# Kernel tuning notes

Hardware: AMD Instinct MI355X
Metric: run time of the kernel (lower is better)

## Reference

```python
import math
import jax, jax.numpy as jnp
import numpy as np

PRED_LEN = 96
K = 32
LOW_FREQ = 1


def setup_inputs() -> dict:
    key = jax.random.key(0)
    x = jax.random.normal(key, (8, 512, 512), dtype=jnp.float32)
    return {"x": x}


def _fourier_forward(x):
    b, t, d = x.shape
    # rFFT over time axis (always fp32, matching torch autocast-disabled block)
    x_freq = jnp.fft.rfft(x.astype(jnp.float32), axis=1)  # (b, t//2+1, d) complex64
    freqs = jnp.fft.rfftfreq(t).astype(jnp.float32)
    if t % 2 == 0:
        x_freq = x_freq[:, LOW_FREQ:-1]
        f = freqs[LOW_FREQ:-1]
    else:
        x_freq = x_freq[:, LOW_FREQ:]
        f = freqs[LOW_FREQ:]
    n_freq = x_freq.shape[1]
    k = min(K, n_freq)

    # top-k |X(f)| independently per (batch, channel): move freq to last axis
    mag = jnp.transpose(jnp.abs(x_freq), (0, 2, 1))          # (b, d, f)
    _, idx = jax.lax.top_k(mag, k)                            # (b, d, k)
    x_freq_t = jnp.transpose(x_freq, (0, 2, 1))               # (b, d, f)
    x_sel = jnp.transpose(jnp.take_along_axis(x_freq_t, idx, axis=2), (0, 2, 1))  # (b, k, d)
    f_sel = jnp.transpose(f[idx], (0, 2, 1))[:, :, None, :]   # (b, k, 1, d)

    # extrapolate: add conjugate (negative) frequencies
    x_full = jnp.concatenate([x_sel, jnp.conj(x_sel)], axis=1)  # (b, 2k, d)
    f_full = jnp.concatenate([f_sel, -f_sel], axis=1)           # (b, 2k, 1, d)
    t_val = jnp.arange(t + PRED_LEN, dtype=jnp.float32)[None, None, :, None]  # (1,1,T,1)
    amp = (jnp.abs(x_full) / t)[:, :, None, :]                  # (b, 2k, 1, d)
    phase = jnp.angle(x_full)[:, :, None, :]                    # (b, 2k, 1, d)
    x_time = amp * jnp.cos(2.0 * math.pi * f_full * t_val + phase)  # (b, 2k, T, d)
    return jnp.sum(x_time, axis=1)                              # (b, t+pred_len, d)


def reference(x):
    return _fourier_forward(x)
```

## Files before the change

### kernel.cpp

```cpp
#include <hip/hip_runtime.h>
#include <math.h>

#define BATCH 8
#define TLEN  512
#define DDIM  512
#define TOUT  608
#define KSEL  32
#define DT    8

#define TWO_PI_OVER_512 0.0122718463030851562f
#define SC (2.0f / 512.0f)

typedef __attribute__((ext_vector_type(8))) short short8;
typedef __attribute__((ext_vector_type(4))) float f32x4;

#define BMT_OFF 0
#define WK_OFF  4194304

__device__ __forceinline__ unsigned short f2bf(float f) {
    unsigned u = __float_as_uint(f);
    return (unsigned short)((u + 0x7FFF + ((u >> 16) & 1)) >> 16);
}

__device__ __constant__ const float CC16[16] = {
     1.f,  0.92387953251128674f,  0.70710678118654752f,  0.38268343236508977f,
     0.f, -0.38268343236508977f, -0.70710678118654752f, -0.92387953251128674f,
    -1.f, -0.92387953251128674f, -0.70710678118654752f, -0.38268343236508977f,
     0.f,  0.38268343236508977f,  0.70710678118654752f,  0.92387953251128674f };
__device__ __constant__ const float SS16[16] = {
     0.f,  0.38268343236508977f,  0.70710678118654752f,  0.92387953251128674f,
     1.f,  0.92387953251128674f,  0.70710678118654752f,  0.38268343236508977f,
     0.f, -0.38268343236508977f, -0.70710678118654752f, -0.92387953251128674f,
    -1.f, -0.92387953251128674f, -0.70710678118654752f, -0.38268343236508977f };

__global__ __launch_bounds__(512, 4) void fft_topk_kernel(const float* __restrict__ x,
                                                          unsigned short* __restrict__ BmT,
                                                          unsigned short* __restrict__ Wk) {
    __shared__ float2 Xl[DT][257];
    __shared__ float  ysr[16 * 33 * 9];
    __shared__ float  ysi[16 * 33 * 9];
    __shared__ float2 tw[512];

    const int tid = threadIdx.x;
    const int bid = blockIdx.x;
    const int b   = bid >> 6;
    const int d0  = ((bid & 7) * 8 + ((bid >> 3) & 7)) * DT;

    {
        float s, c;
        sincosf((float)tid * TWO_PI_OVER_512, &s, &c);
        tw[tid] = make_float2(c, s);
    }

    {
        const int h   = tid >> 8;
        const int rem = tid & 255;
        const int aA  = rem >> 3;
        const int dA  = rem & 7;
        const float* xb = x + ((size_t)b * TLEN + aA) * DDIM + d0 + dA;
        float xv[16];
        #pragma unroll
        for (int c = 0; c < 16; ++c)
            xv[c] = xb[(size_t)c * 32 * DDIM];

        #pragma unroll
        for (int qn = 0; qn < 8; ++qn) {
            const int q = qn + 8 * h;
            float sr = 0.f, si = 0.f;
            #pragma unroll
            for (int c = 0; c < 16; ++c) {
                const int n = (c * q) & 15;
                sr = fmaf(xv[c],  CC16[n], sr);
                si = fmaf(xv[c], -SS16[n], si);
            }
            ysr[(q * 33 + aA) * 9 + dA] = sr;
            ysi[(q * 33 + aA) * 9 + dA] = si;
        }
    }
    __syncthreads();

    {
        const int ahalf = tid & 1;
        const int dB    = (tid >> 1) & 7;
        const int kk    = tid >> 4;
        const int qq    = kk & 15;

        const int ybase = (qq * 33 + ahalf * 16) * 9 + dB;
        float Yr_[16], Yi_[16], Pr_[16], Pi_[16];
        #pragma unroll
        for (int aa = 0; aa < 16; ++aa) {
            Yr_[aa] = ysr[ybase + aa * 9];
            Yi_[aa] = ysi[ybase + aa * 9];
        }
        #pragma unroll
        for (int aa = 0; aa < 16; ++aa) {
            const int arow = ahalf * 16 + aa;
            float2 w = tw[(arow * kk) & 511];
            Pr_[aa] = w.x;
            Pi_[aa] = -w.y;
        }

        float ar[8] = {}, ai[8] = {};
        #pragma unroll
        for (int aa = 0; aa < 16; ++aa) {
            float zr = Yr_[aa] * Pr_[aa] - Yi_[aa] * Pi_[aa];
            float zi = Yr_[aa] * Pi_[aa] + Yi_[aa] * Pr_[aa];
            #pragma unroll
            for (int u = 0; u < 8; ++u) {
                const int n = (aa * u) & 15;
                ar[u] = fmaf(zr, CC16[n], fmaf(zi,  SS16[n], ar[u]));
                ai[u] = fmaf(zi, CC16[n], fmaf(-zr, SS16[n], ai[u]));
            }
        }

        #pragma unroll
        for (int u = 0; u < 8; ++u) {
            ar[u] += __shfl_xor(ar[u], 1);
            ai[u] += __shfl_xor(ai[u], 1);
        }
        #pragma unroll
        for (int v = 0; v < 4; ++v) {
            const int u = ahalf * 4 + v;
            Xl[dB][kk + 32 * u] = make_float2(ar[u], ai[u]);
        }
    }
    __syncthreads();

    if (tid < 256) {
        float2 w = tw[(bid * tid) & 511];
        unsigned val = (unsigned)f2bf(w.x * SC) | ((unsigned)f2bf(-w.y * SC) << 16);
        *(unsigned*)&Wk[((size_t)bid << 9) + 2 * tid] = val;
    }

    {
        const int l  = tid & 63;
        const int dd = tid >> 6;
        const unsigned long long below = ((unsigned long long)1 << l) - 1;

        float zr[4], zi[4];
        unsigned vb[4];
        int mm[4];
        #pragma unroll
        for (int s = 0; s < 4; ++s) {
            int m = 1 + l + 64 * s;
            mm[s] = m;
            if (m <= 255) {
                float2 z = Xl[dd][m];
                zr[s] = z.x; zi[s] = z.y;
                vb[s] = __float_as_uint(fmaf(z.x, z.x, z.y * z.y));
            } else { zr[s] = 0.f; zi[s] = 0.f; vb[s] = 0u; }
        }

        unsigned tau = 0;
        for (int bit = 30; bit >= 0; --bit) {
            unsigned cand = tau | (1u << bit);
            int cnt = __popcll(__ballot(vb[0] >= cand))
                    + __popcll(__ballot(vb[1] >= cand))
                    + __popcll(__ballot(vb[2] >= cand))
                    + __popcll(__ballot(vb[3] >= cand));
            if (cnt >= KSEL) tau = cand;
        }

        unsigned long long beq[4];
        int cgt = 0;
        #pragma unroll
        for (int s = 0; s < 4; ++s) {
            beq[s] = __ballot(vb[s] == tau);
            cgt += __popcll(__ballot(vb[s] > tau));
        }
        const int need = KSEL - cgt;

        unsigned short* Brow = BmT + ((size_t)(b * DDIM + d0 + dd) << 9);
        int be = 0;
        #pragma unroll
        for (int s = 0; s < 4; ++s) {
            bool keep = (vb[s] > tau);
            if (vb[s] == tau) {
                int r = be + __popcll(beq[s] & below);
                keep = (r < need);
            }
            be += __popcll(beq[s]);
            unsigned val = keep ? ((unsigned)f2bf(zr[s]) | ((unsigned)f2bf(zi[s]) << 16)) : 0u;
            int mi = mm[s] & 255;
            *(unsigned*)(Brow + 2 * mi) = val;
        }
    }
}

__global__ __launch_bounds__(512, 4) void gemm_kernel(const unsigned short* __restrict__ Wk,
                                                      const unsigned short* __restrict__ BmT,
                                                      float* __restrict__ out) {
    __shared__ unsigned short Al[64][136];
    __shared__ unsigned short Bl[64][136];

    const int tid = threadIdx.x;
    const int bid = blockIdx.x;
    const int bt  = bid >> 6;
    const int b   = (bid >> 3) & 7;
    const int bd  = bid & 7;

    const int wid  = tid >> 6;
    const int l    = tid & 63;
    const int wm   = wid & 3;
    const int wn   = wid >> 2;
    const int lrow = l & 15;
    const int lk8  = (l >> 4) * 8;

    const int srow = tid >> 3;
    const int soff = (tid & 7) * 8;

    const unsigned short* Wrow = Wk  + (size_t)(bt * 64 + srow) * 512 + soff;
    const unsigned short* Brow = BmT + ((size_t)(b * DDIM + bd * 64 + srow)) * 512 + soff;

    f32x4 acc0 = {0.f, 0.f, 0.f, 0.f};
    f32x4 acc1 = {0.f, 0.f, 0.f, 0.f};

    uint4 av0 = *(const uint4*)(Wrow);
    uint4 av1 = *(const uint4*)(Wrow + 64);
    uint4 bv0 = *(const uint4*)(Brow);
    uint4 bv1 = *(const uint4*)(Brow + 64);

    for (int kc = 0; kc < 512; kc += 128) {
        __syncthreads();
        *(uint4*)&Al[srow][soff]      = av0;
        *(uint4*)&Al[srow][soff + 64] = av1;
        *(uint4*)&Bl[srow][soff]      = bv0;
        *(uint4*)&Bl[srow][soff + 64] = bv1;
        __syncthreads();

        if (kc + 128 < 512) {
            av0 = *(const uint4*)(Wrow + kc + 128);
            av1 = *(const uint4*)(Wrow + kc + 192);
            bv0 = *(const uint4*)(Brow + kc + 128);
            bv1 = *(const uint4*)(Brow + kc + 192);
        }

        #pragma unroll
        for (int ks = 0; ks < 4; ++ks) {
            short8 af  = *(const short8*)&Al[wm * 16 + lrow][ks * 32 + lk8];
            short8 bf0 = *(const short8*)&Bl[wn * 32 + lrow][ks * 32 + lk8];
            short8 bf1 = *(const short8*)&Bl[wn * 32 + 16 + lrow][ks * 32 + lk8];
            acc0 = __builtin_amdgcn_mfma_f32_16x16x32_bf16(af, bf0, acc0, 0, 0, 0);
            acc1 = __builtin_amdgcn_mfma_f32_16x16x32_bf16(af, bf1, acc1, 0, 0, 0);
        }
    }

    const int tg = bt * 64 + wm * 16 + (l >> 4) * 4;
    const int dg = bd * 64 + wn * 32 + (l & 15);
    float* ob = out + (size_t)b * TOUT * DDIM;
    #pragma unroll
    for (int r = 0; r < 4; ++r) {
        const int t = tg + r;
        ob[(size_t)t * DDIM + dg]      = acc0[r];
        ob[(size_t)t * DDIM + dg + 16] = acc1[r];
        if (t < 96) {
            ob[(size_t)(t + 512) * DDIM + dg]      = acc0[r];
            ob[(size_t)(t + 512) * DDIM + dg + 16] = acc1[r];
        }
    }
}

extern "C" void kernel_launch(void* const* d_in, const int* in_sizes, int n_in,
                              void* d_out, int out_size, void* d_ws, size_t ws_size,
                              hipStream_t stream) {
    const float* x   = (const float*)d_in[0];
    float*       out = (float*)d_out;
    unsigned short* BmT = (unsigned short*)((char*)d_ws + BMT_OFF);
    unsigned short* Wk  = (unsigned short*)((char*)d_ws + WK_OFF);

    fft_topk_kernel<<<BATCH * 64, 512, 0, stream>>>(x, BmT, Wk);
    gemm_kernel<<<BATCH * 64, 512, 0, stream>>>(Wk, BmT, out);
}
```

Baseline: 26.63 us.

## Stage input tile via coalesced float4 loads into shared memory; radix-4 top-k threshold search

```diff
diff --git a/kernel.cpp b/kernel.cpp
--- a/kernel.cpp
+++ b/kernel.cpp
@@ -36,10 +36,12 @@
 __global__ __launch_bounds__(512, 4) void fft_topk_kernel(const float* __restrict__ x,
                                                           unsigned short* __restrict__ BmT,
                                                           unsigned short* __restrict__ Wk) {
-    __shared__ float2 Xl[DT][257];
-    __shared__ float  ysr[16 * 33 * 9];
-    __shared__ float  ysi[16 * 33 * 9];
-    __shared__ float2 tw[512];
+    __shared__ __align__(16) unsigned char smem[58560];
+    float2* Xl  = (float2*)smem;
+    float*  xs  = (float*)smem;
+    float*  ysr = (float*)(smem + 16448);
+    float*  ysi = (float*)(smem + 35456);
+    float2* tw  = (float2*)(smem + 54464);
 
     const int tid = threadIdx.x;
     const int bid = blockIdx.x;
@@ -53,15 +55,23 @@
     }
 
     {
+        const float* xr = x + ((size_t)b * TLEN + tid) * DDIM + d0;
+        float4 lo = *(const float4*)(xr);
+        float4 hi = *(const float4*)(xr + 4);
+        *(float4*)&xs[tid * 8]     = lo;
+        *(float4*)&xs[tid * 8 + 4] = hi;
+    }
+    __syncthreads();
+
+    {
         const int h   = tid >> 8;
         const int rem = tid & 255;
         const int aA  = rem >> 3;
         const int dA  = rem & 7;
-        const float* xb = x + ((size_t)b * TLEN + aA) * DDIM + d0 + dA;
         float xv[16];
         #pragma unroll
         for (int c = 0; c < 16; ++c)
-            xv[c] = xb[(size_t)c * 32 * DDIM];
+            xv[c] = xs[(aA + 32 * c) * 8 + dA];
 
         #pragma unroll
         for (int qn = 0; qn < 8; ++qn) {
@@ -121,7 +131,7 @@
         #pragma unroll
         for (int v = 0; v < 4; ++v) {
             const int u = ahalf * 4 + v;
-            Xl[dB][kk + 32 * u] = make_float2(ar[u], ai[u]);
+            Xl[dB * 257 + kk + 32 * u] = make_float2(ar[u], ai[u]);
         }
     }
     __syncthreads();
@@ -145,20 +155,31 @@
             int m = 1 + l + 64 * s;
             mm[s] = m;
             if (m <= 255) {
-                float2 z = Xl[dd][m];
+                float2 z = Xl[dd * 257 + m];
                 zr[s] = z.x; zi[s] = z.y;
                 vb[s] = __float_as_uint(fmaf(z.x, z.x, z.y * z.y));
             } else { zr[s] = 0.f; zi[s] = 0.f; vb[s] = 0u; }
         }
 
         unsigned tau = 0;
-        for (int bit = 30; bit >= 0; --bit) {
-            unsigned cand = tau | (1u << bit);
-            int cnt = __popcll(__ballot(vb[0] >= cand))
-                    + __popcll(__ballot(vb[1] >= cand))
-                    + __popcll(__ballot(vb[2] >= cand))
-                    + __popcll(__ballot(vb[3] >= cand));
-            if (cnt >= KSEL) tau = cand;
+        #pragma unroll
+        for (int bit = 29; bit >= 1; bit -= 2) {
+            const unsigned c1 = tau | (1u << bit);
+            const unsigned c2 = tau | (2u << bit);
+            const unsigned c3 = tau | (3u << bit);
+            int n1 = __popcll(__ballot(vb[0] >= c1)) + __popcll(__ballot(vb[1] >= c1))
+                   + __popcll(__ballot(vb[2] >= c1)) + __popcll(__ballot(vb[3] >= c1));
+            int n2 = __popcll(__ballot(vb[0] >= c2)) + __popcll(__ballot(vb[1] >= c2))
+                   + __popcll(__ballot(vb[2] >= c2)) + __popcll(__ballot(vb[3] >= c2));
+            int n3 = __popcll(__ballot(vb[0] >= c3)) + __popcll(__ballot(vb[1] >= c3))
+                   + __popcll(__ballot(vb[2] >= c3)) + __popcll(__ballot(vb[3] >= c3));
+            tau = (n3 >= KSEL) ? c3 : (n2 >= KSEL) ? c2 : (n1 >= KSEL) ? c1 : tau;
+        }
+        {
+            const unsigned c = tau | 1u;
+            int n = __popcll(__ballot(vb[0] >= c)) + __popcll(__ballot(vb[1] >= c))
+                  + __popcll(__ballot(vb[2] >= c)) + __popcll(__ballot(vb[3] >= c));
+            if (n >= KSEL) tau = c;
         }
 
         unsigned long long beq[4];
```

Measured after the change: 26.79 us. No clear change (+0.6%).
